# Performance work log

Measured on AMD Instinct MI355X. Metric: run time of the kernel, lower is better.

The kernel has to match this reference:

```python
import jax, jax.numpy as jnp
import numpy as np

WEIGHT_CE = 1.0
WEIGHT_DICE = 1.0
EPS = 1e-10
SMOOTH = 1e-5


def setup_inputs() -> dict:
    key = jax.random.key(0)
    k1, k2 = jax.random.split(key)
    B, N, H, W, D = 2, 8, 128, 128, 128
    logits = jax.random.normal(k1, (B, N, H, W, D), dtype=jnp.float32)
    pred = jax.nn.softmax(logits, axis=1)  # module expects softmaxed preds
    target = jax.random.randint(k2, (B, 1, H, W, D), 0, N, dtype=jnp.int32)
    return {"pred": pred, "target": target}


def reference(pred, target):
    # pred: (B, N, H, W, D) softmax probs; target: (B, 1, H, W, D) int labels
    B, N = pred.shape[0], pred.shape[1]
    t = target[:, 0]  # (B, H, W, D)

    # --- CE part (faithful to the original's cross-batch one-hot bug) ---
    # loss[b2, hwd] = -sum_b sum_c 1[t[b2,hwd]==c] * log(pred[b,c,hwd]+eps)
    logp_sum = jnp.sum(jnp.log(pred + EPS), axis=0)  # (N, H, W, D)
    gathered = jnp.take_along_axis(
        jnp.broadcast_to(logp_sum[None], (B,) + logp_sum.shape),
        t[:, None], axis=1)[:, 0]  # (B, H, W, D)
    celoss = -jnp.mean(gathered) / B

    # --- MONAI DiceLoss(softmax=False, to_onehot_y=True), defaults ---
    oh = (t[:, None] == jnp.arange(N, dtype=t.dtype)[None, :, None, None, None]).astype(pred.dtype)  # (B,N,H,W,D)
    inter = jnp.sum(oh * pred, axis=(2, 3, 4))   # (B, N)
    ground_o = jnp.sum(oh, axis=(2, 3, 4))       # (B, N)
    pred_o = jnp.sum(pred, axis=(2, 3, 4))       # (B, N)
    dice = jnp.mean(1.0 - (2.0 * inter + SMOOTH) / (ground_o + pred_o + SMOOTH))

    return WEIGHT_CE * celoss + WEIGHT_DICE * dice
```

## Files before the change

### kernel.cpp

```cpp
#include <hip/hip_runtime.h>

#define S_VOX (128*128*128)
#define QV (S_VOX/4)
#define EPSF 1e-10f
#define SMOOTHF 1e-5f

#define NACC 49

__device__ __forceinline__ float wave_reduce(float v) {
#pragma unroll
    for (int off = 32; off > 0; off >>= 1)
        v += __shfl_down(v, off, 64);
    return v;
}

__global__ __launch_bounds__(256) void dice_main(const float* __restrict__ pred,
                                                 const int* __restrict__ tgt,
                                                 float* __restrict__ ws) {
    const float4* p4 = (const float4*)pred;
    const int4*   t4 = (const int4*)tgt;

    float ce = 0.f;
    float inter[2][8];
    float po[2][8];
    int   gc[2][8];
#pragma unroll
    for (int b = 0; b < 2; b++)
#pragma unroll
        for (int n = 0; n < 8; n++) { inter[b][n] = 0.f; po[b][n] = 0.f; gc[b][n] = 0; }

    const int tid    = blockIdx.x * blockDim.x + threadIdx.x;
    const int stride = gridDim.x * blockDim.x;

    for (int q = tid; q < QV; q += stride) {
        const int4 t0 = t4[q];
        const int4 t1 = t4[QV + q];
#pragma unroll
        for (int n = 0; n < 8; n++) {
            const float4 a = p4[n * QV + q];
            const float4 b = p4[(8 + n) * QV + q];

            po[0][n] += (a.x + a.y) + (a.z + a.w);
            po[1][n] += (b.x + b.y) + (b.z + b.w);

#define VOXEL(pa, pb, ta, tb)                                              \
            {                                                              \
                float lg = __logf((pa) + EPSF) + __logf((pb) + EPSF);      \
                int m0 = ((ta) == n);                                      \
                int m1 = ((tb) == n);                                      \
                ce += lg * (float)(m0 + m1);                               \
                inter[0][n] += m0 ? (pa) : 0.f;                            \
                inter[1][n] += m1 ? (pb) : 0.f;                            \
                gc[0][n] += m0;                                            \
                gc[1][n] += m1;                                            \
            }
            VOXEL(a.x, b.x, t0.x, t1.x)
            VOXEL(a.y, b.y, t0.y, t1.y)
            VOXEL(a.z, b.z, t0.z, t1.z)
            VOXEL(a.w, b.w, t0.w, t1.w)
#undef VOXEL
        }
    }

    float acc[NACC];
    acc[0] = ce;
#pragma unroll
    for (int b = 0; b < 2; b++)
#pragma unroll
        for (int n = 0; n < 8; n++) {
            acc[1  + b * 8 + n] = inter[b][n];
            acc[17 + b * 8 + n] = (float)gc[b][n];
            acc[33 + b * 8 + n] = po[b][n];
        }

    __shared__ float red[4][NACC];
    const int lane = threadIdx.x & 63;
    const int wave = threadIdx.x >> 6;
#pragma unroll
    for (int i = 0; i < NACC; i++) {
        float v = wave_reduce(acc[i]);
        if (lane == 0) red[wave][i] = v;
    }
    __syncthreads();
    if (threadIdx.x < NACC) {
        float s = red[0][threadIdx.x] + red[1][threadIdx.x] +
                  red[2][threadIdx.x] + red[3][threadIdx.x];
        atomicAdd(&ws[threadIdx.x], s);
    }
}

__global__ void dice_finalize(const float* __restrict__ ws, float* __restrict__ out) {
    const int i = threadIdx.x;
    float term = 0.f;
    if (i < 16) {
        float inter = ws[1 + i];
        float g     = ws[17 + i];
        float p     = ws[33 + i];
        term = 1.0f - (2.0f * inter + SMOOTHF) / (g + p + SMOOTHF);
    }
    term = wave_reduce(term);
    if (i == 0) {
        float celoss = -ws[0] / (4.0f * (float)S_VOX);
        out[0] = celoss + term * (1.0f / 16.0f);
    }
}

extern "C" void kernel_launch(void* const* d_in, const int* in_sizes, int n_in,
                              void* d_out, int out_size, void* d_ws, size_t ws_size,
                              hipStream_t stream) {
    const float* pred = (const float*)d_in[0];
    const int*   tgt  = (const int*)d_in[1];
    float* ws  = (float*)d_ws;
    float* out = (float*)d_out;

    hipMemsetAsync(ws, 0, NACC * sizeof(float), stream);
    dice_main<<<1024, 256, 0, stream>>>(pred, tgt, ws);
    dice_finalize<<<1, 64, 0, stream>>>(ws, out);
}
```

Measured before the change: 230.3 us.

## Split work per batch and gather pred before taking a single log

Result: faster. 223.3 us (-3.0%).

```diff
diff --git a/kernel.cpp b/kernel.cpp
--- a/kernel.cpp
+++ b/kernel.cpp
@@ -17,75 +17,83 @@
 __global__ __launch_bounds__(256) void dice_main(const float* __restrict__ pred,
                                                  const int* __restrict__ tgt,
                                                  float* __restrict__ ws) {
-    const float4* p4 = (const float4*)pred;
-    const int4*   t4 = (const int4*)tgt;
+    const int b   = blockIdx.x & 1;
+    const int bid = blockIdx.x >> 1;
+    const int nbb = gridDim.x >> 1;
+
+    const float4* p4   = (const float4*)pred + (size_t)b * 8u * (size_t)QV;
+    const int4*   town = (const int4*)tgt + (size_t)b * (size_t)QV;
+    const int4*   toth = (const int4*)tgt + (size_t)(1 - b) * (size_t)QV;
 
     float ce = 0.f;
-    float inter[2][8];
-    float po[2][8];
-    int   gc[2][8];
+    float inter[8], po[8];
+    int   gc[8];
 #pragma unroll
-    for (int b = 0; b < 2; b++)
-#pragma unroll
-        for (int n = 0; n < 8; n++) { inter[b][n] = 0.f; po[b][n] = 0.f; gc[b][n] = 0; }
+    for (int n = 0; n < 8; n++) { inter[n] = 0.f; po[n] = 0.f; gc[n] = 0; }
 
-    const int tid    = blockIdx.x * blockDim.x + threadIdx.x;
-    const int stride = gridDim.x * blockDim.x;
+    const int tid0   = bid * blockDim.x + threadIdx.x;
+    const int stride = nbb * blockDim.x;
 
-    for (int q = tid; q < QV; q += stride) {
-        const int4 t0 = t4[q];
-        const int4 t1 = t4[QV + q];
+    for (int q = tid0; q < QV; q += stride) {
+        const int4 t0 = town[q];
+        const int4 t1 = toth[q];
+        float so0 = 0.f, so1 = 0.f, so2 = 0.f, so3 = 0.f;
+        float st0 = 0.f, st1 = 0.f, st2 = 0.f, st3 = 0.f;
 #pragma unroll
         for (int n = 0; n < 8; n++) {
-            const float4 a = p4[n * QV + q];
-            const float4 b = p4[(8 + n) * QV + q];
+            const float4 p = p4[(size_t)n * QV + q];
+            po[n] += (p.x + p.y) + (p.z + p.w);
 
-            po[0][n] += (a.x + a.y) + (a.z + a.w);
-            po[1][n] += (b.x + b.y) + (b.z + b.w);
-
-#define VOXEL(pa, pb, ta, tb)                                              \
-            {                                                              \
-                float lg = __logf((pa) + EPSF) + __logf((pb) + EPSF);      \
-                int m0 = ((ta) == n);                                      \
-                int m1 = ((tb) == n);                                      \
-                ce += lg * (float)(m0 + m1);                               \
-                inter[0][n] += m0 ? (pa) : 0.f;                            \
-                inter[1][n] += m1 ? (pb) : 0.f;                            \
-                gc[0][n] += m0;                                            \
-                gc[1][n] += m1;                                            \
+#define SLOT(pv, ta, tb, so, st)                                        \
+            {                                                           \
+                const bool m0 = ((ta) == n);                            \
+                const bool m1 = ((tb) == n);                            \
+                const float v0 = m0 ? (pv) : 0.f;                       \
+                inter[n] += v0;                                         \
+                so += v0;                                               \
+                st += m1 ? (pv) : 0.f;                                  \
+                gc[n] += (int)m0;                                       \
             }
-            VOXEL(a.x, b.x, t0.x, t1.x)
-            VOXEL(a.y, b.y, t0.y, t1.y)
-            VOXEL(a.z, b.z, t0.z, t1.z)
-            VOXEL(a.w, b.w, t0.w, t1.w)
-#undef VOXEL
+            SLOT(p.x, t0.x, t1.x, so0, st0)
+            SLOT(p.y, t0.y, t1.y, so1, st1)
+            SLOT(p.z, t0.z, t1.z, so2, st2)
+            SLOT(p.w, t0.w, t1.w, so3, st3)
+#undef SLOT
         }
+        ce += __logf(so0 + EPSF) + __logf(st0 + EPSF);
+        ce += __logf(so1 + EPSF) + __logf(st1 + EPSF);
+        ce += __logf(so2 + EPSF) + __logf(st2 + EPSF);
+        ce += __logf(so3 + EPSF) + __logf(st3 + EPSF);
     }
 
-    float acc[NACC];
+    __shared__ float red[4][25];
+    const int lane = threadIdx.x & 63;
+    const int wave = threadIdx.x >> 6;
+
+    float acc[25];
     acc[0] = ce;
 #pragma unroll
-    for (int b = 0; b < 2; b++)
+    for (int n = 0; n < 8; n++) {
+        acc[1 + n]  = inter[n];
+        acc[9 + n]  = po[n];
+        acc[17 + n] = (float)gc[n];
+    }
 #pragma unroll
-        for (int n = 0; n < 8; n++) {
-            acc[1  + b * 8 + n] = inter[b][n];
-            acc[17 + b * 8 + n] = (float)gc[b][n];
-            acc[33 + b * 8 + n] = po[b][n];
-        }
-
-    __shared__ float red[4][NACC];
-    const int lane = threadIdx.x & 63;
-    const int wave = threadIdx.x >> 6;
-#pragma unroll
-    for (int i = 0; i < NACC; i++) {
+    for (int i = 0; i < 25; i++) {
         float v = wave_reduce(acc[i]);
         if (lane == 0) red[wave][i] = v;
     }
     __syncthreads();
-    if (threadIdx.x < NACC) {
-        float s = red[0][threadIdx.x] + red[1][threadIdx.x] +
-                  red[2][threadIdx.x] + red[3][threadIdx.x];
-        atomicAdd(&ws[threadIdx.x], s);
+
+    const int i = threadIdx.x;
+    if (i < 25) {
+        float s = red[0][i] + red[1][i] + red[2][i] + red[3][i];
+        int dst;
+        if (i == 0)       dst = 0;
+        else if (i <= 8)  dst = 1  + b * 8 + (i - 1);
+        else if (i <= 16) dst = 33 + b * 8 + (i - 9);
+        else              dst = 17 + b * 8 + (i - 17);
+        atomicAdd(&ws[dst], s);
     }
 }
 
@@ -114,6 +122,6 @@
     float* out = (float*)d_out;
 
     hipMemsetAsync(ws, 0, NACC * sizeof(float), stream);
-    dice_main<<<1024, 256, 0, stream>>>(pred, tgt, ws);
+    dice_main<<<2048, 256, 0, stream>>>(pred, tgt, ws);
     dice_finalize<<<1, 64, 0, stream>>>(ws, out);
 }
```
